# Kernel optimization log

Hardware: AMD Instinct MI355X
Metric: run time of the kernel (lower is better)

Reference implementation:

```python
import jax, jax.numpy as jnp
import numpy as np

N, D, E = 10000, 64, 32768   # nodes, padded degree, target edges
F, H, O = 64, 256, 1         # in_channels, hidden_channels, out_channels


def _linear_init(key, fin, fout):
    kw, kb = jax.random.split(key)
    s = 1.0 / np.sqrt(fin)
    w = jax.random.uniform(kw, (fin, fout), jnp.float32, -s, s)
    b = jax.random.uniform(kb, (fout,), jnp.float32, -s, s)
    return w, b


def setup_inputs() -> dict:
    key = jax.random.key(0)
    ks = jax.random.split(key, 12)
    x = jax.random.normal(ks[0], (N, F), jnp.float32)
    adj_nbr = jax.random.randint(ks[1], (N, D), 0, N)          # padded neighbor lists
    tar_ei = jax.random.randint(ks[2], (2, E), 0, N)           # target edges
    xcn_w1, xcn_b1 = _linear_init(ks[3], F, H)
    xcn_w2, xcn_b2 = _linear_init(ks[4], H, H)
    xcn_w3, xcn_b3 = _linear_init(ks[5], H, H)
    xij_w1, xij_b1 = _linear_init(ks[6], F, H)
    xij_w2, xij_b2 = _linear_init(ks[7], H, H)
    lin_w1, lin_b1 = _linear_init(ks[8], H, H)
    lin_w2, lin_b2 = _linear_init(ks[9], H, O)
    beta = jnp.ones((1,), jnp.float32)
    return dict(x=x, adj_nbr=adj_nbr, tar_ei=tar_ei, beta=beta,
                xcn_w1=xcn_w1, xcn_b1=xcn_b1, xcn_w2=xcn_w2, xcn_b2=xcn_b2,
                xcn_w3=xcn_w3, xcn_b3=xcn_b3,
                xij_w1=xij_w1, xij_b1=xij_b1, xij_w2=xij_w2, xij_b2=xij_b2,
                lin_w1=lin_w1, lin_b1=lin_b1, lin_w2=lin_w2, lin_b2=lin_b2)


def reference(x, adj_nbr, tar_ei, beta,
              xcn_w1, xcn_b1, xcn_w2, xcn_b2, xcn_w3, xcn_b3,
              xij_w1, xij_b1, xij_w2, xij_b2,
              lin_w1, lin_b1, lin_w2, lin_b2):
    relu = jax.nn.relu
    i, j = tar_ei[0], tar_ei[1]
    # adjoverlap: common-neighbor intersection of rows i and j of the adjacency
    ni = adj_nbr[i]                                   # [E, D] neighbors of i
    nj = adj_nbr[j]                                   # [E, D] neighbors of j
    cm = (ni[:, :, None] == nj[:, None, :]).any(-1)   # [E, D] ni[a] in N(j)?
    # spmm_add(cn, x): sum features of common neighbors per target edge
    xcn = jnp.einsum('ed,edf->ef', cm.astype(x.dtype), x[ni])  # [E, F]
    # xijlin(xi * xj): Linear -> ReLU -> Linear
    xij = x[i] * x[j]
    h_ij = relu(xij @ xij_w1 + xij_b1) @ xij_w2 + xij_b2
    # xcnlin(xcn): Linear -> ReLU -> Linear -> ReLU -> Linear
    h_cn = relu(xcn @ xcn_w1 + xcn_b1)
    h_cn = relu(h_cn @ xcn_w2 + xcn_b2)
    h_cn = h_cn @ xcn_w3 + xcn_b3
    # lin(xcnlin(xcn) * beta + xij): Linear -> ReLU -> Linear
    h = relu((h_cn * beta + h_ij) @ lin_w1 + lin_b1)
    return h @ lin_w2 + lin_b2                        # [E, O]
```

## Files before the change

### kernel.cpp

```cpp
#include <hip/hip_runtime.h>

#define NNODES 10000
#define DDEG   64
#define NEDGES 32768
#define FIN    64
#define HID    256

typedef __attribute__((ext_vector_type(8))) __bf16 bf16x8;
typedef __attribute__((ext_vector_type(4))) float  f32x4;

__device__ __forceinline__ unsigned short f2bf(float f) {
    unsigned x = __float_as_uint(f);
    return (unsigned short)((x + 0x7FFFu + ((x >> 16) & 1u)) >> 16);
}
__device__ __forceinline__ float b2f(unsigned short u) {
    return __uint_as_float(((unsigned)u) << 16);
}

#define OFF_XIJ1 0
#define OFF_XIJ2 16384
#define OFF_XCN1 81920
#define OFF_XCN2 98304
#define OFF_XCN3 163840
#define OFF_LIN1 229376
#define WT_TOTAL 294912
#define NTILES   36

__host__ __device__ constexpr int tile_off(int t) {
    return t < 2  ? OFF_XIJ1 + t * 8192
         : t < 10 ? OFF_XIJ2 + (t - 2) * 8192
         : t < 12 ? OFF_XCN1 + (t - 10) * 8192
         : t < 20 ? OFF_XCN2 + (t - 12) * 8192
         : t < 28 ? OFF_XCN3 + (t - 20) * 8192
         :          OFF_LIN1 + (t - 28) * 8192;
}

__device__ __forceinline__ void gll16(const unsigned short* g, unsigned short* l) {
    __builtin_amdgcn_global_load_lds(
        (const __attribute__((address_space(1))) unsigned int*)g,
        (__attribute__((address_space(3))) unsigned int*)l, 16, 0, 0);
}
__device__ __forceinline__ void stage_tile(const unsigned short* g, unsigned short* l,
                                           int tid, int wv) {
#pragma unroll
    for (int c = 0; c < 2; ++c)
        gll16(g + c * 4096 + tid * 8, l + c * 4096 + wv * 512);
}

__global__ __launch_bounds__(256) void edge_prep_k(const float* __restrict__ x,
                                                   const int* __restrict__ adj,
                                                   const int* __restrict__ tar,
                                                   const float* __restrict__ xij_w1,
                                                   const float* __restrict__ xij_w2,
                                                   const float* __restrict__ xcn_w1,
                                                   const float* __restrict__ xcn_w2,
                                                   const float* __restrict__ xcn_w3,
                                                   const float* __restrict__ lin_w1,
                                                   unsigned short* __restrict__ WT,
                                                   unsigned short* __restrict__ xij_g,
                                                   unsigned short* __restrict__ xcn_g) {
    const int wv   = threadIdx.x >> 6;
    const int lane = threadIdx.x & 63;
    const int e    = blockIdx.x * 4 + wv;

    int i = tar[e];
    int j = tar[NEDGES + e];
    int ni = adj[i * DDEG + lane];
    int nj = adj[j * DDEG + lane];
    float xi = x[i * FIN + lane];
    float xj = x[j * FIN + lane];

    bool found = false;
#pragma unroll
    for (int b = 0; b < 64; ++b)
        found |= (ni == (int)__builtin_amdgcn_readlane(nj, b));
    unsigned long long m = __ballot(found);

    float acc = 0.f;
    while (m) {
        int a = __ffsll(m) - 1;
        m &= m - 1;
        int r = (int)__builtin_amdgcn_readlane(ni, a);
        acc += x[r * FIN + lane];
    }
    int sl = lane ^ ((e & 7) << 3);
    xij_g[(size_t)e * FIN + sl] = f2bf(xi * xj);
    xcn_g[(size_t)e * FIN + sl] = f2bf(acc);

    if (blockIdx.x < WT_TOTAL / 256) {
        int idx = blockIdx.x * 256 + threadIdx.x;
        const float* src;
        int r;
        if (idx < OFF_XIJ2)      { r = idx - OFF_XIJ1; src = xij_w1; }
        else if (idx < OFF_XCN1) { r = idx - OFF_XIJ2; src = xij_w2; }
        else if (idx < OFF_XCN2) { r = idx - OFF_XCN1; src = xcn_w1; }
        else if (idx < OFF_XCN3) { r = idx - OFF_XCN2; src = xcn_w2; }
        else if (idx < OFF_LIN1) { r = idx - OFF_XCN3; src = xcn_w3; }
        else                     { r = idx - OFF_LIN1; src = lin_w1; }
        int kb  = r >> 13;
        int n   = (r & 8191) >> 5;
        int klo = r & 31;
        WT[idx] = f2bf(src[(kb * 32 + klo) * HID + n]);
    }
}

template <int T0, int NT, int LDA>
__device__ __forceinline__ void run_phase(const unsigned short* As,
                                          unsigned short* ring,
                                          const unsigned short* __restrict__ WT,
                                          int lr, int lg, int col0, int r0,
                                          int tid, int wv, f32x4 acc[2][4]) {
#pragma unroll
    for (int m = 0; m < 2; ++m)
#pragma unroll
        for (int n = 0; n < 4; ++n) acc[m][n] = (f32x4){0.f, 0.f, 0.f, 0.f};
    const int sw = (lr & 7) << 3;
#pragma unroll
    for (int s = 0; s < NT; ++s) {
        if (T0 + s + 1 < NTILES)
            asm volatile("s_waitcnt vmcnt(2) lgkmcnt(0)" ::: "memory");
        else
            asm volatile("s_waitcnt vmcnt(0) lgkmcnt(0)" ::: "memory");
        __builtin_amdgcn_s_barrier();
        const unsigned short* cur = ring + ((T0 + s) & 1) * 8192;
        bf16x8 a[2], b[4];
#pragma unroll
        for (int n = 0; n < 4; ++n)
            b[n] = *reinterpret_cast<const bf16x8*>(&cur[(col0 + n * 16 + lr) * 32 + 8 * lg]);
#pragma unroll
        for (int m = 0; m < 2; ++m)
            a[m] = *reinterpret_cast<const bf16x8*>(
                &As[(r0 + m * 16 + lr) * LDA + ((s * 32 + 8 * lg) ^ sw)]);
        __builtin_amdgcn_s_setprio(1);
#pragma unroll
        for (int m = 0; m < 2; ++m)
#pragma unroll
            for (int n = 0; n < 4; ++n)
                acc[m][n] = __builtin_amdgcn_mfma_f32_16x16x32_bf16(a[m], b[n], acc[m][n], 0, 0, 0);
        __builtin_amdgcn_s_setprio(0);
        asm volatile("s_waitcnt lgkmcnt(0)" ::: "memory");
        __builtin_amdgcn_s_barrier();
        if (T0 + s + 2 < NTILES)
            stage_tile(WT + tile_off(T0 + s + 2), ring + ((T0 + s) & 1) * 8192, tid, wv);
    }
}

__global__ __launch_bounds__(512, 2) void mlp_k(const unsigned short* __restrict__ xij_g,
                                                const unsigned short* __restrict__ xcn_g,
                                                const unsigned short* __restrict__ WT,
                                                const float* __restrict__ xij_b1,
                                                const float* __restrict__ xij_b2,
                                                const float* __restrict__ xcn_b1,
                                                const float* __restrict__ xcn_b2,
                                                const float* __restrict__ xcn_b3,
                                                const float* __restrict__ lin_b1,
                                                const float* __restrict__ lin_w2,
                                                const float* __restrict__ lin_b2,
                                                const float* __restrict__ beta,
                                                float* __restrict__ out) {
    __shared__ unsigned short sXij[64 * 64];
    __shared__ unsigned short sXcn[64 * 64];
    __shared__ unsigned short sH[64 * 256];
    __shared__ unsigned short sB[2 * 8192];

    const int tid  = threadIdx.x;
    const int wv   = tid >> 6;
    const int lane = tid & 63;
    const int lr   = lane & 15;
    const int lg   = lane >> 4;
    const int r0   = (wv >> 2) * 32;
    const int col0 = (wv & 3) * 64;
    const int row0 = blockIdx.x * 64;

    gll16(xij_g + (size_t)row0 * FIN + tid * 8, sXij + wv * 512);
    gll16(xcn_g + (size_t)row0 * FIN + tid * 8, sXcn + wv * 512);
    stage_tile(WT + tile_off(0), sB, tid, wv);
    stage_tile(WT + tile_off(1), sB + 8192, tid, wv);
    const float betaf = beta[0];

    f32x4 acc[2][4];
    float bl[4];

    run_phase<0, 2, 64>(sXij, sB, WT, lr, lg, col0, r0, tid, wv, acc);
#pragma unroll
    for (int n = 0; n < 4; ++n) bl[n] = xij_b1[col0 + n * 16 + lr];
#pragma unroll
    for (int m = 0; m < 2; ++m)
#pragma unroll
        for (int n = 0; n < 4; ++n)
#pragma unroll
            for (int i = 0; i < 4; ++i) {
                int row = r0 + m * 16 + 4 * lg + i;
                int col = col0 + n * 16 + lr;
                sH[row * HID + (col ^ ((row & 7) << 3))] = f2bf(fmaxf(acc[m][n][i] + bl[n], 0.f));
            }

    run_phase<2, 8, 256>(sH, sB, WT, lr, lg, col0, r0, tid, wv, acc);
#pragma unroll
    for (int n = 0; n < 4; ++n) bl[n] = xij_b2[col0 + n * 16 + lr];
    unsigned hij_lo[2][4], hij_hi[2][4];
#pragma unroll
    for (int m = 0; m < 2; ++m)
#pragma unroll
        for (int n = 0; n < 4; ++n) {
            hij_lo[m][n] = ((unsigned)f2bf(acc[m][n][1] + bl[n]) << 16) | f2bf(acc[m][n][0] + bl[n]);
            hij_hi[m][n] = ((unsigned)f2bf(acc[m][n][3] + bl[n]) << 16) | f2bf(acc[m][n][2] + bl[n]);
        }

    run_phase<10, 2, 64>(sXcn, sB, WT, lr, lg, col0, r0, tid, wv, acc);
#pragma unroll
    for (int n = 0; n < 4; ++n) bl[n] = xcn_b1[col0 + n * 16 + lr];
#pragma unroll
    for (int m = 0; m < 2; ++m)
#pragma unroll
        for (int n = 0; n < 4; ++n)
#pragma unroll
            for (int i = 0; i < 4; ++i) {
                int row = r0 + m * 16 + 4 * lg + i;
                int col = col0 + n * 16 + lr;
                sH[row * HID + (col ^ ((row & 7) << 3))] = f2bf(fmaxf(acc[m][n][i] + bl[n], 0.f));
            }

    run_phase<12, 8, 256>(sH, sB, WT, lr, lg, col0, r0, tid, wv, acc);
#pragma unroll
    for (int n = 0; n < 4; ++n) bl[n] = xcn_b2[col0 + n * 16 + lr];
#pragma unroll
    for (int m = 0; m < 2; ++m)
#pragma unroll
        for (int n = 0; n < 4; ++n)
#pragma unroll
            for (int i = 0; i < 4; ++i) {
                int row = r0 + m * 16 + 4 * lg + i;
                int col = col0 + n * 16 + lr;
                sH[row * HID + (col ^ ((row & 7) << 3))] = f2bf(fmaxf(acc[m][n][i] + bl[n], 0.f));
            }

    run_phase<20, 8, 256>(sH, sB, WT, lr, lg, col0, r0, tid, wv, acc);
#pragma unroll
    for (int n = 0; n < 4; ++n) bl[n] = xcn_b3[col0 + n * 16 + lr];
#pragma unroll
    for (int m = 0; m < 2; ++m)
#pragma unroll
        for (int n = 0; n < 4; ++n) {
            float h0 = b2f((unsigned short)(hij_lo[m][n] & 0xFFFF));
            float h1 = b2f((unsigned short)(hij_lo[m][n] >> 16));
            float h2 = b2f((unsigned short)(hij_hi[m][n] & 0xFFFF));
            float h3 = b2f((unsigned short)(hij_hi[m][n] >> 16));
            float v0 = (acc[m][n][0] + bl[n]) * betaf + h0;
            float v1 = (acc[m][n][1] + bl[n]) * betaf + h1;
            float v2 = (acc[m][n][2] + bl[n]) * betaf + h2;
            float v3 = (acc[m][n][3] + bl[n]) * betaf + h3;
            int rb = r0 + m * 16 + 4 * lg;
            int col = col0 + n * 16 + lr;
            sH[(rb + 0) * HID + (col ^ (((rb + 0) & 7) << 3))] = f2bf(v0);
            sH[(rb + 1) * HID + (col ^ (((rb + 1) & 7) << 3))] = f2bf(v1);
            sH[(rb + 2) * HID + (col ^ (((rb + 2) & 7) << 3))] = f2bf(v2);
            sH[(rb + 3) * HID + (col ^ (((rb + 3) & 7) << 3))] = f2bf(v3);
        }

    run_phase<28, 8, 256>(sH, sB, WT, lr, lg, col0, r0, tid, wv, acc);
#pragma unroll
    for (int n = 0; n < 4; ++n) bl[n] = lin_b1[col0 + n * 16 + lr];
    float w2l[4];
#pragma unroll
    for (int n = 0; n < 4; ++n) w2l[n] = lin_w2[col0 + n * 16 + lr];
    float* sRed = (float*)sXij;
#pragma unroll
    for (int m = 0; m < 2; ++m) {
        float p[4] = {0.f, 0.f, 0.f, 0.f};
#pragma unroll
        for (int n = 0; n < 4; ++n)
#pragma unroll
            for (int i = 0; i < 4; ++i)
                p[i] += fmaxf(acc[m][n][i] + bl[n], 0.f) * w2l[n];
#pragma unroll
        for (int i = 0; i < 4; ++i) {
            float s = p[i];
            s += __shfl_xor(s, 1);
            s += __shfl_xor(s, 2);
            s += __shfl_xor(s, 4);
            s += __shfl_xor(s, 8);
            if (lr == 0) sRed[(wv & 3) * 64 + r0 + m * 16 + 4 * lg + i] = s;
        }
    }
    __syncthreads();
    if (tid < 64)
        out[row0 + tid] = sRed[tid] + sRed[64 + tid] + sRed[128 + tid] + sRed[192 + tid] + lin_b2[0];
}

extern "C" void kernel_launch(void* const* d_in, const int* in_sizes, int n_in,
                              void* d_out, int out_size, void* d_ws, size_t ws_size,
                              hipStream_t stream) {
    const float* x      = (const float*)d_in[0];
    const int*   adj    = (const int*)d_in[1];
    const int*   tar    = (const int*)d_in[2];
    const float* beta   = (const float*)d_in[3];
    const float* xcn_w1 = (const float*)d_in[4];
    const float* xcn_b1 = (const float*)d_in[5];
    const float* xcn_w2 = (const float*)d_in[6];
    const float* xcn_b2 = (const float*)d_in[7];
    const float* xcn_w3 = (const float*)d_in[8];
    const float* xcn_b3 = (const float*)d_in[9];
    const float* xij_w1 = (const float*)d_in[10];
    const float* xij_b1 = (const float*)d_in[11];
    const float* xij_w2 = (const float*)d_in[12];
    const float* xij_b2 = (const float*)d_in[13];
    const float* lin_w1 = (const float*)d_in[14];
    const float* lin_b1 = (const float*)d_in[15];
    const float* lin_w2 = (const float*)d_in[16];
    const float* lin_b2 = (const float*)d_in[17];

    unsigned short* WT    = (unsigned short*)d_ws;
    unsigned short* xij_g = (unsigned short*)((char*)d_ws + 589824);
    unsigned short* xcn_g = (unsigned short*)((char*)d_ws + 4784128);

    edge_prep_k<<<NEDGES / 4, 256, 0, stream>>>(x, adj, tar,
                                                xij_w1, xij_w2, xcn_w1, xcn_w2, xcn_w3, lin_w1,
                                                WT, xij_g, xcn_g);
    mlp_k<<<NEDGES / 64, 512, 0, stream>>>(xij_g, xcn_g, WT,
                                           xij_b1, xij_b2, xcn_b1, xcn_b2, xcn_b3,
                                           lin_b1, lin_w2, lin_b2, beta, (float*)d_out);
}
```

Measured before the change: 67.29 us.

## Fuse edge gather into MLP kernel with 128-row tiles and triple-buffered weights

Moves the common-neighbor intersection and feature gather into the MLP kernel, so per-edge bf16 inputs are written straight to shared memory instead of round-tripping through global workspace. The weight conversion now runs as its own small kernel. Each block now handles 128 edges with a 4x4 MFMA tile per wave, which halves the weight re-streaming per edge, and the weight ring grows to three buffers so one barrier per k-step can be dropped. The costs are one block per CU (about 112KB of LDS), 256 blocks that underfill the GPU, and a serial 16-edge gather loop per wave before any MFMA work starts.

```diff
diff --git a/kernel.cpp b/kernel.cpp
--- a/kernel.cpp
+++ b/kernel.cpp
@@ -35,6 +35,28 @@
          :          OFF_LIN1 + (t - 28) * 8192;
 }
 
+__global__ __launch_bounds__(256) void prep_k(const float* __restrict__ xij_w1,
+                                              const float* __restrict__ xij_w2,
+                                              const float* __restrict__ xcn_w1,
+                                              const float* __restrict__ xcn_w2,
+                                              const float* __restrict__ xcn_w3,
+                                              const float* __restrict__ lin_w1,
+                                              unsigned short* __restrict__ WT) {
+    int idx = blockIdx.x * 256 + threadIdx.x;
+    const float* src;
+    int r;
+    if (idx < OFF_XIJ2)      { r = idx - OFF_XIJ1; src = xij_w1; }
+    else if (idx < OFF_XCN1) { r = idx - OFF_XIJ2; src = xij_w2; }
+    else if (idx < OFF_XCN2) { r = idx - OFF_XCN1; src = xcn_w1; }
+    else if (idx < OFF_XCN3) { r = idx - OFF_XCN2; src = xcn_w2; }
+    else if (idx < OFF_LIN1) { r = idx - OFF_XCN3; src = xcn_w3; }
+    else                     { r = idx - OFF_LIN1; src = lin_w1; }
+    int kb  = r >> 13;
+    int n   = (r & 8191) >> 5;
+    int klo = r & 31;
+    WT[idx] = f2bf(src[(kb * 32 + klo) * HID + n]);
+}
+
 __device__ __forceinline__ void gll16(const unsigned short* g, unsigned short* l) {
     __builtin_amdgcn_global_load_lds(
         (const __attribute__((address_space(1))) unsigned int*)g,
@@ -45,63 +67,6 @@
 #pragma unroll
     for (int c = 0; c < 2; ++c)
         gll16(g + c * 4096 + tid * 8, l + c * 4096 + wv * 512);
-}
-
-__global__ __launch_bounds__(256) void edge_prep_k(const float* __restrict__ x,
-                                                   const int* __restrict__ adj,
-                                                   const int* __restrict__ tar,
-                                                   const float* __restrict__ xij_w1,
-                                                   const float* __restrict__ xij_w2,
-                                                   const float* __restrict__ xcn_w1,
-                                                   const float* __restrict__ xcn_w2,
-                                                   const float* __restrict__ xcn_w3,
-                                                   const float* __restrict__ lin_w1,
-                                                   unsigned short* __restrict__ WT,
-                                                   unsigned short* __restrict__ xij_g,
-                                                   unsigned short* __restrict__ xcn_g) {
-    const int wv   = threadIdx.x >> 6;
-    const int lane = threadIdx.x & 63;
-    const int e    = blockIdx.x * 4 + wv;
-
-    int i = tar[e];
-    int j = tar[NEDGES + e];
-    int ni = adj[i * DDEG + lane];
-    int nj = adj[j * DDEG + lane];
-    float xi = x[i * FIN + lane];
-    float xj = x[j * FIN + lane];
-
-    bool found = false;
-#pragma unroll
-    for (int b = 0; b < 64; ++b)
-        found |= (ni == (int)__builtin_amdgcn_readlane(nj, b));
-    unsigned long long m = __ballot(found);
-
-    float acc = 0.f;
-    while (m) {
-        int a = __ffsll(m) - 1;
-        m &= m - 1;
-        int r = (int)__builtin_amdgcn_readlane(ni, a);
-        acc += x[r * FIN + lane];
-    }
-    int sl = lane ^ ((e & 7) << 3);
-    xij_g[(size_t)e * FIN + sl] = f2bf(xi * xj);
-    xcn_g[(size_t)e * FIN + sl] = f2bf(acc);
-
-    if (blockIdx.x < WT_TOTAL / 256) {
-        int idx = blockIdx.x * 256 + threadIdx.x;
-        const float* src;
-        int r;
-        if (idx < OFF_XIJ2)      { r = idx - OFF_XIJ1; src = xij_w1; }
-        else if (idx < OFF_XCN1) { r = idx - OFF_XIJ2; src = xij_w2; }
-        else if (idx < OFF_XCN2) { r = idx - OFF_XCN1; src = xcn_w1; }
-        else if (idx < OFF_XCN3) { r = idx - OFF_XCN2; src = xcn_w2; }
-        else if (idx < OFF_LIN1) { r = idx - OFF_XCN3; src = xcn_w3; }
-        else                     { r = idx - OFF_LIN1; src = lin_w1; }
-        int kb  = r >> 13;
-        int n   = (r & 8191) >> 5;
-        int klo = r & 31;
-        WT[idx] = f2bf(src[(kb * 32 + klo) * HID + n]);
-    }
 }
 
 template <int T0, int NT, int LDA>
@@ -109,83 +74,120 @@
                                           unsigned short* ring,
                                           const unsigned short* __restrict__ WT,
                                           int lr, int lg, int col0, int r0,
-                                          int tid, int wv, f32x4 acc[2][4]) {
-#pragma unroll
-    for (int m = 0; m < 2; ++m)
+                                          int tid, int wv, f32x4 acc[4][4]) {
+#pragma unroll
+    for (int m = 0; m < 4; ++m)
 #pragma unroll
         for (int n = 0; n < 4; ++n) acc[m][n] = (f32x4){0.f, 0.f, 0.f, 0.f};
     const int sw = (lr & 7) << 3;
 #pragma unroll
     for (int s = 0; s < NT; ++s) {
-        if (T0 + s + 1 < NTILES)
+        const int t = T0 + s;
+        if (t < NTILES - 1)
             asm volatile("s_waitcnt vmcnt(2) lgkmcnt(0)" ::: "memory");
         else
             asm volatile("s_waitcnt vmcnt(0) lgkmcnt(0)" ::: "memory");
         __builtin_amdgcn_s_barrier();
-        const unsigned short* cur = ring + ((T0 + s) & 1) * 8192;
-        bf16x8 a[2], b[4];
+        const unsigned short* cur = ring + (t % 3) * 8192;
+        bf16x8 a[4], b[4];
 #pragma unroll
         for (int n = 0; n < 4; ++n)
             b[n] = *reinterpret_cast<const bf16x8*>(&cur[(col0 + n * 16 + lr) * 32 + 8 * lg]);
 #pragma unroll
-        for (int m = 0; m < 2; ++m)
+        for (int m = 0; m < 4; ++m)
             a[m] = *reinterpret_cast<const bf16x8*>(
                 &As[(r0 + m * 16 + lr) * LDA + ((s * 32 + 8 * lg) ^ sw)]);
         __builtin_amdgcn_s_setprio(1);
 #pragma unroll
-        for (int m = 0; m < 2; ++m)
+        for (int m = 0; m < 4; ++m)
 #pragma unroll
             for (int n = 0; n < 4; ++n)
                 acc[m][n] = __builtin_amdgcn_mfma_f32_16x16x32_bf16(a[m], b[n], acc[m][n], 0, 0, 0);
         __builtin_amdgcn_s_setprio(0);
-        asm volatile("s_waitcnt lgkmcnt(0)" ::: "memory");
-        __builtin_amdgcn_s_barrier();
-        if (T0 + s + 2 < NTILES)
-            stage_tile(WT + tile_off(T0 + s + 2), ring + ((T0 + s) & 1) * 8192, tid, wv);
+        if (t + 2 < NTILES)
+            stage_tile(WT + tile_off(t + 2), ring + ((t + 2) % 3) * 8192, tid, wv);
     }
 }
 
-__global__ __launch_bounds__(512, 2) void mlp_k(const unsigned short* __restrict__ xij_g,
-                                                const unsigned short* __restrict__ xcn_g,
-                                                const unsigned short* __restrict__ WT,
-                                                const float* __restrict__ xij_b1,
-                                                const float* __restrict__ xij_b2,
-                                                const float* __restrict__ xcn_b1,
-                                                const float* __restrict__ xcn_b2,
-                                                const float* __restrict__ xcn_b3,
-                                                const float* __restrict__ lin_b1,
-                                                const float* __restrict__ lin_w2,
-                                                const float* __restrict__ lin_b2,
-                                                const float* __restrict__ beta,
-                                                float* __restrict__ out) {
-    __shared__ unsigned short sXij[64 * 64];
-    __shared__ unsigned short sXcn[64 * 64];
-    __shared__ unsigned short sH[64 * 256];
-    __shared__ unsigned short sB[2 * 8192];
+__global__ __launch_bounds__(512, 1) void fused_k(const float* __restrict__ x,
+                                                  const int* __restrict__ adj,
+                                                  const int* __restrict__ tar,
+                                                  const unsigned short* __restrict__ WT,
+                                                  const float* __restrict__ xij_b1,
+                                                  const float* __restrict__ xij_b2,
+                                                  const float* __restrict__ xcn_b1,
+                                                  const float* __restrict__ xcn_b2,
+                                                  const float* __restrict__ xcn_b3,
+                                                  const float* __restrict__ lin_b1,
+                                                  const float* __restrict__ lin_w2,
+                                                  const float* __restrict__ lin_b2,
+                                                  const float* __restrict__ beta,
+                                                  float* __restrict__ out) {
+    __shared__ unsigned short sXij[128 * 64];
+    __shared__ unsigned short sXcn[128 * 64];
+    __shared__ unsigned short sH[128 * 256];
+    __shared__ unsigned short sB[3 * 8192];
 
     const int tid  = threadIdx.x;
     const int wv   = tid >> 6;
     const int lane = tid & 63;
     const int lr   = lane & 15;
     const int lg   = lane >> 4;
-    const int r0   = (wv >> 2) * 32;
+    const int r0   = (wv >> 2) * 64;
     const int col0 = (wv & 3) * 64;
-    const int row0 = blockIdx.x * 64;
-
-    gll16(xij_g + (size_t)row0 * FIN + tid * 8, sXij + wv * 512);
-    gll16(xcn_g + (size_t)row0 * FIN + tid * 8, sXcn + wv * 512);
+    const int row0 = blockIdx.x * 128;
+
     stage_tile(WT + tile_off(0), sB, tid, wv);
     stage_tile(WT + tile_off(1), sB + 8192, tid, wv);
     const float betaf = beta[0];
 
-    f32x4 acc[2][4];
+    {
+        const int e0 = row0 + wv * 16;
+        int   ic = tar[e0];
+        int   jc = tar[NEDGES + e0];
+        int   ni_c = adj[ic * DDEG + lane];
+        int   nj_c = adj[jc * DDEG + lane];
+        float xi_c = x[ic * FIN + lane];
+        float xj_c = x[jc * FIN + lane];
+        for (int t = 0; t < 16; ++t) {
+            int ni = ni_c, nj = nj_c;
+            float xi = xi_c, xj = xj_c;
+            if (t < 15) {
+                int e = e0 + t + 1;
+                int i2 = tar[e];
+                int j2 = tar[NEDGES + e];
+                ni_c = adj[i2 * DDEG + lane];
+                nj_c = adj[j2 * DDEG + lane];
+                xi_c = x[i2 * FIN + lane];
+                xj_c = x[j2 * FIN + lane];
+            }
+            bool found = false;
+#pragma unroll
+            for (int b = 0; b < 64; ++b)
+                found |= (ni == (int)__builtin_amdgcn_readlane(nj, b));
+            unsigned long long m = __ballot(found);
+            float acc = 0.f;
+            while (m) {
+                int a = __ffsll(m) - 1;
+                m &= m - 1;
+                int r = (int)__builtin_amdgcn_readlane(ni, a);
+                acc += x[r * FIN + lane];
+            }
+            int el = wv * 16 + t;
+            int sidx = el * FIN + (lane ^ ((el & 7) << 3));
+            sXij[sidx] = f2bf(xi * xj);
+            sXcn[sidx] = f2bf(acc);
+        }
+    }
+
+    f32x4 acc[4][4];
     float bl[4];
 
     run_phase<0, 2, 64>(sXij, sB, WT, lr, lg, col0, r0, tid, wv, acc);
 #pragma unroll
     for (int n = 0; n < 4; ++n) bl[n] = xij_b1[col0 + n * 16 + lr];
 #pragma unroll
-    for (int m = 0; m < 2; ++m)
+    for (int m = 0; m < 4; ++m)
 #pragma unroll
         for (int n = 0; n < 4; ++n)
 #pragma unroll
@@ -198,9 +200,9 @@
     run_phase<2, 8, 256>(sH, sB, WT, lr, lg, col0, r0, tid, wv, acc);
 #pragma unroll
     for (int n = 0; n < 4; ++n) bl[n] = xij_b2[col0 + n * 16 + lr];
-    unsigned hij_lo[2][4], hij_hi[2][4];
-#pragma unroll
-    for (int m = 0; m < 2; ++m)
+    unsigned hij_lo[4][4], hij_hi[4][4];
+#pragma unroll
+    for (int m = 0; m < 4; ++m)
 #pragma unroll
         for (int n = 0; n < 4; ++n) {
             hij_lo[m][n] = ((unsigned)f2bf(acc[m][n][1] + bl[n]) << 16) | f2bf(acc[m][n][0] + bl[n]);
@@ -211,7 +213,7 @@
 #pragma unroll
     for (int n = 0; n < 4; ++n) bl[n] = xcn_b1[col0 + n * 16 + lr];
 #pragma unroll
-    for (int m = 0; m < 2; ++m)
+    for (int m = 0; m < 4; ++m)
 #pragma unroll
         for (int n = 0; n < 4; ++n)
 #pragma unroll
@@ -222,10 +224,12 @@
             }
 
     run_phase<12, 8, 256>(sH, sB, WT, lr, lg, col0, r0, tid, wv, acc);
+    asm volatile("s_waitcnt lgkmcnt(0)" ::: "memory");
+    __builtin_amdgcn_s_barrier();
 #pragma unroll
     for (int n = 0; n < 4; ++n) bl[n] = xcn_b2[col0 + n * 16 + lr];
 #pragma unroll
-    for (int m = 0; m < 2; ++m)
+    for (int m = 0; m < 4; ++m)
 #pragma unroll
         for (int n = 0; n < 4; ++n)
 #pragma unroll
@@ -236,10 +240,12 @@
             }
 
     run_phase<20, 8, 256>(sH, sB, WT, lr, lg, col0, r0, tid, wv, acc);
+    asm volatile("s_waitcnt lgkmcnt(0)" ::: "memory");
+    __builtin_amdgcn_s_barrier();
 #pragma unroll
     for (int n = 0; n < 4; ++n) bl[n] = xcn_b3[col0 + n * 16 + lr];
 #pragma unroll
-    for (int m = 0; m < 2; ++m)
+    for (int m = 0; m < 4; ++m)
 #pragma unroll
         for (int n = 0; n < 4; ++n) {
             float h0 = b2f((unsigned short)(hij_lo[m][n] & 0xFFFF));
@@ -266,7 +272,7 @@
     for (int n = 0; n < 4; ++n) w2l[n] = lin_w2[col0 + n * 16 + lr];
     float* sRed = (float*)sXij;
 #pragma unroll
-    for (int m = 0; m < 2; ++m) {
+    for (int m = 0; m < 4; ++m) {
         float p[4] = {0.f, 0.f, 0.f, 0.f};
 #pragma unroll
         for (int n = 0; n < 4; ++n)
@@ -280,12 +286,12 @@
             s += __shfl_xor(s, 2);
             s += __shfl_xor(s, 4);
             s += __shfl_xor(s, 8);
-            if (lr == 0) sRed[(wv & 3) * 64 + r0 + m * 16 + 4 * lg + i] = s;
+            if (lr == 0) sRed[(wv & 3) * 128 + r0 + m * 16 + 4 * lg + i] = s;
         }
     }
     __syncthreads();
-    if (tid < 64)
-        out[row0 + tid] = sRed[tid] + sRed[64 + tid] + sRed[128 + tid] + sRed[192 + tid] + lin_b2[0];
+    if (tid < 128)
+        out[row0 + tid] = sRed[tid] + sRed[128 + tid] + sRed[256 + tid] + sRed[384 + tid] + lin_b2[0];
 }
 
 extern "C" void kernel_launch(void* const* d_in, const int* in_sizes, int n_in,
@@ -310,14 +316,10 @@
     const float* lin_w2 = (const float*)d_in[16];
     const float* lin_b2 = (const float*)d_in[17];
 
-    unsigned short* WT    = (unsigned short*)d_ws;
-    unsigned short* xij_g = (unsigned short*)((char*)d_ws + 589824);
-    unsigned short* xcn_g = (unsigned short*)((char*)d_ws + 4784128);
-
-    edge_prep_k<<<NEDGES / 4, 256, 0, stream>>>(x, adj, tar,
-                                                xij_w1, xij_w2, xcn_w1, xcn_w2, xcn_w3, lin_w1,
-                                                WT, xij_g, xcn_g);
-    mlp_k<<<NEDGES / 64, 512, 0, stream>>>(xij_g, xcn_g, WT,
-                                           xij_b1, xij_b2, xcn_b1, xcn_b2, xcn_b3,
-                                           lin_b1, lin_w2, lin_b2, beta, (float*)d_out);
-}
+    unsigned short* WT = (unsigned short*)d_ws;
+
+    prep_k<<<WT_TOTAL / 256, 256, 0, stream>>>(xij_w1, xij_w2, xcn_w1, xcn_w2, xcn_w3, lin_w1, WT);
+    fused_k<<<NEDGES / 128, 512, 0, stream>>>(x, adj, tar, WT,
+                                              xij_b1, xij_b2, xcn_b1, xcn_b2, xcn_b3,
+                                              lin_b1, lin_w2, lin_b2, beta, (float*)d_out);
+}
```

Result: slower. 72.43 us (+7.6%).

## Stage weight tiles in pairs through a triple-buffered LDS ring

Applied to the files above, without the earlier changes.

Weight staging now moves two K-tiles per step into a three-slot LDS ring instead of one tile into a two-slot ring. Each step therefore needs only one barrier, down from two, and the prefetch for the next pair is issued right after that barrier. The aim is to halve synchronisation and deepen the prefetch. In exchange LDS use grows to 96 KB for the weight ring, so launch bounds drop to one block per CU. Explicit barriers are added after phases whose outputs overwrite sH, since the trailing barrier no longer protects it.

```diff
diff --git a/kernel.cpp b/kernel.cpp
--- a/kernel.cpp
+++ b/kernel.cpp
@@ -25,6 +25,7 @@
 #define OFF_LIN1 229376
 #define WT_TOTAL 294912
 #define NTILES   36
+#define NPAIRS   18
 
 __host__ __device__ constexpr int tile_off(int t) {
     return t < 2  ? OFF_XIJ1 + t * 8192
@@ -40,11 +41,17 @@
         (const __attribute__((address_space(1))) unsigned int*)g,
         (__attribute__((address_space(3))) unsigned int*)l, 16, 0, 0);
 }
-__device__ __forceinline__ void stage_tile(const unsigned short* g, unsigned short* l,
-                                           int tid, int wv) {
-#pragma unroll
-    for (int c = 0; c < 2; ++c)
-        gll16(g + c * 4096 + tid * 8, l + c * 4096 + wv * 512);
+__device__ __forceinline__ void stage_pair(const unsigned short* __restrict__ WT, int p,
+                                           unsigned short* ring, int tid, int wv) {
+    const unsigned short* src = WT + tile_off(2 * p);
+    unsigned short* dst = ring + (p % 3) * 16384;
+#pragma unroll
+    for (int c = 0; c < 4; ++c)
+        gll16(src + c * 4096 + tid * 8, dst + c * 4096 + wv * 512);
+}
+__device__ __forceinline__ void stage_act(const unsigned short* g, unsigned short* l,
+                                          int tid, int wv) {
+    gll16(g + tid * 8, l + wv * 512);
 }
 
 __global__ __launch_bounds__(256) void edge_prep_k(const float* __restrict__ x,
@@ -104,7 +111,7 @@
     }
 }
 
-template <int T0, int NT, int LDA>
+template <int G0, int NSS, int LDA>
 __device__ __forceinline__ void run_phase(const unsigned short* As,
                                           unsigned short* ring,
                                           const unsigned short* __restrict__ WT,
@@ -116,36 +123,39 @@
         for (int n = 0; n < 4; ++n) acc[m][n] = (f32x4){0.f, 0.f, 0.f, 0.f};
     const int sw = (lr & 7) << 3;
 #pragma unroll
-    for (int s = 0; s < NT; ++s) {
-        if (T0 + s + 1 < NTILES)
-            asm volatile("s_waitcnt vmcnt(2) lgkmcnt(0)" ::: "memory");
+    for (int ss = 0; ss < NSS; ++ss) {
+        const int g = G0 + ss;
+        if (g + 1 < NPAIRS)
+            asm volatile("s_waitcnt vmcnt(4) lgkmcnt(0)" ::: "memory");
         else
             asm volatile("s_waitcnt vmcnt(0) lgkmcnt(0)" ::: "memory");
         __builtin_amdgcn_s_barrier();
-        const unsigned short* cur = ring + ((T0 + s) & 1) * 8192;
-        bf16x8 a[2], b[4];
-#pragma unroll
-        for (int n = 0; n < 4; ++n)
-            b[n] = *reinterpret_cast<const bf16x8*>(&cur[(col0 + n * 16 + lr) * 32 + 8 * lg]);
-#pragma unroll
-        for (int m = 0; m < 2; ++m)
-            a[m] = *reinterpret_cast<const bf16x8*>(
-                &As[(r0 + m * 16 + lr) * LDA + ((s * 32 + 8 * lg) ^ sw)]);
-        __builtin_amdgcn_s_setprio(1);
-#pragma unroll
-        for (int m = 0; m < 2; ++m)
+        if (g + 2 < NPAIRS)
+            stage_pair(WT, g + 2, ring, tid, wv);
+#pragma unroll
+        for (int half = 0; half < 2; ++half) {
+            const int kk = (ss * 2 + half) * 32;
+            const unsigned short* cur = ring + (g % 3) * 16384 + half * 8192;
+            bf16x8 a[2], b[4];
 #pragma unroll
             for (int n = 0; n < 4; ++n)
-                acc[m][n] = __builtin_amdgcn_mfma_f32_16x16x32_bf16(a[m], b[n], acc[m][n], 0, 0, 0);
-        __builtin_amdgcn_s_setprio(0);
-        asm volatile("s_waitcnt lgkmcnt(0)" ::: "memory");
-        __builtin_amdgcn_s_barrier();
-        if (T0 + s + 2 < NTILES)
-            stage_tile(WT + tile_off(T0 + s + 2), ring + ((T0 + s) & 1) * 8192, tid, wv);
+                b[n] = *reinterpret_cast<const bf16x8*>(&cur[(col0 + n * 16 + lr) * 32 + 8 * lg]);
+#pragma unroll
+            for (int m = 0; m < 2; ++m)
+                a[m] = *reinterpret_cast<const bf16x8*>(
+                    &As[(r0 + m * 16 + lr) * LDA + ((kk + 8 * lg) ^ sw)]);
+            __builtin_amdgcn_s_setprio(1);
+#pragma unroll
+            for (int m = 0; m < 2; ++m)
+#pragma unroll
+                for (int n = 0; n < 4; ++n)
+                    acc[m][n] = __builtin_amdgcn_mfma_f32_16x16x32_bf16(a[m], b[n], acc[m][n], 0, 0, 0);
+            __builtin_amdgcn_s_setprio(0);
+        }
     }
 }
 
-__global__ __launch_bounds__(512, 2) void mlp_k(const unsigned short* __restrict__ xij_g,
+__global__ __launch_bounds__(512, 1) void mlp_k(const unsigned short* __restrict__ xij_g,
                                                 const unsigned short* __restrict__ xcn_g,
                                                 const unsigned short* __restrict__ WT,
                                                 const float* __restrict__ xij_b1,
@@ -161,7 +171,7 @@
     __shared__ unsigned short sXij[64 * 64];
     __shared__ unsigned short sXcn[64 * 64];
     __shared__ unsigned short sH[64 * 256];
-    __shared__ unsigned short sB[2 * 8192];
+    __shared__ unsigned short sB[6 * 8192];
 
     const int tid  = threadIdx.x;
     const int wv   = tid >> 6;
@@ -172,16 +182,16 @@
     const int col0 = (wv & 3) * 64;
     const int row0 = blockIdx.x * 64;
 
-    gll16(xij_g + (size_t)row0 * FIN + tid * 8, sXij + wv * 512);
-    gll16(xcn_g + (size_t)row0 * FIN + tid * 8, sXcn + wv * 512);
-    stage_tile(WT + tile_off(0), sB, tid, wv);
-    stage_tile(WT + tile_off(1), sB + 8192, tid, wv);
+    stage_act(xij_g + (size_t)row0 * FIN, sXij, tid, wv);
+    stage_act(xcn_g + (size_t)row0 * FIN, sXcn, tid, wv);
+    stage_pair(WT, 0, sB, tid, wv);
+    stage_pair(WT, 1, sB, tid, wv);
     const float betaf = beta[0];
 
     f32x4 acc[2][4];
     float bl[4];
 
-    run_phase<0, 2, 64>(sXij, sB, WT, lr, lg, col0, r0, tid, wv, acc);
+    run_phase<0, 1, 64>(sXij, sB, WT, lr, lg, col0, r0, tid, wv, acc);
 #pragma unroll
     for (int n = 0; n < 4; ++n) bl[n] = xij_b1[col0 + n * 16 + lr];
 #pragma unroll
@@ -195,7 +205,7 @@
                 sH[row * HID + (col ^ ((row & 7) << 3))] = f2bf(fmaxf(acc[m][n][i] + bl[n], 0.f));
             }
 
-    run_phase<2, 8, 256>(sH, sB, WT, lr, lg, col0, r0, tid, wv, acc);
+    run_phase<1, 4, 256>(sH, sB, WT, lr, lg, col0, r0, tid, wv, acc);
 #pragma unroll
     for (int n = 0; n < 4; ++n) bl[n] = xij_b2[col0 + n * 16 + lr];
     unsigned hij_lo[2][4], hij_hi[2][4];
@@ -207,7 +217,7 @@
             hij_hi[m][n] = ((unsigned)f2bf(acc[m][n][3] + bl[n]) << 16) | f2bf(acc[m][n][2] + bl[n]);
         }
 
-    run_phase<10, 2, 64>(sXcn, sB, WT, lr, lg, col0, r0, tid, wv, acc);
+    run_phase<5, 1, 64>(sXcn, sB, WT, lr, lg, col0, r0, tid, wv, acc);
 #pragma unroll
     for (int n = 0; n < 4; ++n) bl[n] = xcn_b1[col0 + n * 16 + lr];
 #pragma unroll
@@ -221,7 +231,9 @@
                 sH[row * HID + (col ^ ((row & 7) << 3))] = f2bf(fmaxf(acc[m][n][i] + bl[n], 0.f));
             }
 
-    run_phase<12, 8, 256>(sH, sB, WT, lr, lg, col0, r0, tid, wv, acc);
+    run_phase<6, 4, 256>(sH, sB, WT, lr, lg, col0, r0, tid, wv, acc);
+    asm volatile("s_waitcnt lgkmcnt(0)" ::: "memory");
+    __builtin_amdgcn_s_barrier();
 #pragma unroll
     for (int n = 0; n < 4; ++n) bl[n] = xcn_b2[col0 + n * 16 + lr];
 #pragma unroll
@@ -235,7 +247,9 @@
                 sH[row * HID + (col ^ ((row & 7) << 3))] = f2bf(fmaxf(acc[m][n][i] + bl[n], 0.f));
             }
 
-    run_phase<20, 8, 256>(sH, sB, WT, lr, lg, col0, r0, tid, wv, acc);
+    run_phase<10, 4, 256>(sH, sB, WT, lr, lg, col0, r0, tid, wv, acc);
+    asm volatile("s_waitcnt lgkmcnt(0)" ::: "memory");
+    __builtin_amdgcn_s_barrier();
 #pragma unroll
     for (int n = 0; n < 4; ++n) bl[n] = xcn_b3[col0 + n * 16 + lr];
 #pragma unroll
@@ -258,7 +272,7 @@
             sH[(rb + 3) * HID + (col ^ (((rb + 3) & 7) << 3))] = f2bf(v3);
         }
 
-    run_phase<28, 8, 256>(sH, sB, WT, lr, lg, col0, r0, tid, wv, acc);
+    run_phase<14, 4, 256>(sH, sB, WT, lr, lg, col0, r0, tid, wv, acc);
 #pragma unroll
     for (int n = 0; n < 4; ++n) bl[n] = lin_b1[col0 + n * 16 + lr];
     float w2l[4];
```

New measurement: 62.69 us. 1.07x faster.
